# Kernel optimization log

Hardware: AMD Instinct MI355X
Metric: run time of the kernel (lower is better)

Reference implementation:

```python
import jax, jax.numpy as jnp
import numpy as np

N = 50000      # nodes
E = 1600000    # edges (before self-loops)
IN = 128       # in_chnl
H = 2          # heads
C = 64         # out_chnl per head
NEG_SLOPE = 0.2


def setup_inputs() -> dict:
    key = jax.random.key(0)
    k1, k2, k3, k4, k5 = jax.random.split(key, 5)
    h_node = jax.random.normal(k1, (N, IN), dtype=jnp.float32)
    edge_index = jax.random.randint(k2, (2, E), 0, N, dtype=jnp.int32)
    s = 1.0 / np.sqrt(IN)
    W = (jax.random.normal(k3, (IN, H * C), dtype=jnp.float32) * s)
    att_src = jax.random.normal(k4, (H, C), dtype=jnp.float32) * s
    att_dst = jax.random.normal(k5, (H, C), dtype=jnp.float32) * s
    bias = jnp.zeros((H * C,), dtype=jnp.float32)
    return {"h_node": h_node, "edge_index": edge_index, "W": W,
            "att_src": att_src, "att_dst": att_dst, "bias": bias}


def reference(h_node, edge_index, W, att_src, att_dst, bias):
    # dropout is identity in eval mode
    src, dst = edge_index[0], edge_index[1]
    # PyG GATConv default: add self-loops
    loops = jnp.arange(N, dtype=src.dtype)
    src = jnp.concatenate([src, loops])
    dst = jnp.concatenate([dst, loops])

    x = (h_node @ W).reshape(N, H, C)              # [N,H,C] projected features
    a_s = jnp.sum(x * att_src, axis=-1)            # [N,H] source attention terms
    a_d = jnp.sum(x * att_dst, axis=-1)            # [N,H] dest attention terms

    e = jax.nn.leaky_relu(a_s[src] + a_d[dst], NEG_SLOPE)        # [E+N,H]
    # segment softmax over edges grouped by destination node
    m = jax.lax.stop_gradient(jax.ops.segment_max(e, dst, num_segments=N))
    ex = jnp.exp(e - m[dst])
    den = jax.ops.segment_sum(ex, dst, num_segments=N)           # [N,H]
    alpha = ex / den[dst]                                        # [E+N,H]

    out = jax.ops.segment_sum(alpha[:, :, None] * x[src], dst, num_segments=N)
    out = out.reshape(N, H * C) + bias             # concat=True -> [N, H*C]
    return jax.nn.elu(out)
```

## Files before the change

kernel.cpp:

```cpp
#include <hip/hip_runtime.h>
#include <hip/hip_fp16.h>

#define NN 50000
#define EE 1600000
#define TOT (EE + NN)
#define INC 128
#define HC 128
#define NEG_SLOPE 0.2f

#define EPB 4096
#define NB1 ((TOT + EPB - 1) / EPB)
#define RNG2 64
#define NR2 ((NN + RNG2 - 1) / RNG2)
#define CAPR2 2624
#define PADC (CAPR2 + 4 * RNG2)
#define PROJB ((NN + 63) / 64)

__device__ __forceinline__ unsigned short f2h(float f) {
    __half h = __float2half(f);
    return __half_as_ushort(h);
}

__device__ __forceinline__ unsigned int packp(float a, float b) {
    typedef __fp16 h2 __attribute__((ext_vector_type(2)));
    union { h2 h; unsigned int u; } cv;
    cv.h = __builtin_amdgcn_cvt_pkrtz(a, b);
    return cv.u;
}

#define LOADW(dst, kk)                                                        \
    _Pragma("unroll") for (int q = 0; q < 4; q++) {                           \
        float4 wv4 = *reinterpret_cast<const float4*>(&W[(size_t)((kk) + q) * HC + j2 * 4]); \
        dst[q][0] = wv4.x; dst[q][1] = wv4.y; dst[q][2] = wv4.z; dst[q][3] = wv4.w; \
    }

#define FMAS(wv, kk)                                                          \
    _Pragma("unroll") for (int r8 = 0; r8 < 8; r8++) {                        \
        const float* hr = hs + (rg * 8 + r8) * INC + (kk);                    \
        float4 hv = *reinterpret_cast<const float4*>(hr);                     \
        _Pragma("unroll") for (int c = 0; c < 4; c++)                         \
            acc[r8][c] += hv.x * wv[0][c] + hv.y * wv[1][c]                   \
                        + hv.z * wv[2][c] + hv.w * wv[3][c];                  \
    }

__device__ __forceinline__ void proj_body(
        char* smem, int pb,
        const float* __restrict__ h, const float* __restrict__ W,
        const float* __restrict__ att_src, const float* __restrict__ att_dst,
        unsigned short* __restrict__ x_h,
        float* __restrict__ a_s, float* __restrict__ a_d) {
    float* hs = (float*)smem;
    const int t = threadIdx.x;
    const int row0 = pb * 64;

    for (int q = t; q < 64 * 32; q += 256) {
        int rr = q >> 5;
        int c4 = (q & 31) << 2;
        int gr = row0 + rr;
        float4 v = (gr < NN) ? *reinterpret_cast<const float4*>(&h[(size_t)gr * INC + c4])
                             : make_float4(0.f, 0.f, 0.f, 0.f);
        *reinterpret_cast<float4*>(&hs[rr * INC + c4]) = v;
    }
    __syncthreads();

    const int j2 = t & 31;
    const int rg = t >> 5;
    float acc[8][4];
#pragma unroll
    for (int r8 = 0; r8 < 8; r8++)
#pragma unroll
        for (int c = 0; c < 4; c++) acc[r8][c] = 0.f;

    float wA[4][4], wB[4][4];
    LOADW(wA, 0)
    for (int k = 0; k < INC; k += 8) {
        LOADW(wB, k + 4)
        FMAS(wA, k)
        if (k + 8 < INC) { LOADW(wA, k + 8) }
        FMAS(wB, k + 4)
    }

#pragma unroll
    for (int r8 = 0; r8 < 8; r8++) {
        int gr = row0 + rg * 8 + r8;
        if (gr < NN) {
            ushort4 sv;
            sv.x = f2h(acc[r8][0]);
            sv.y = f2h(acc[r8][1]);
            sv.z = f2h(acc[r8][2]);
            sv.w = f2h(acc[r8][3]);
            *reinterpret_cast<ushort4*>(&x_h[(size_t)gr * HC + j2 * 4]) = sv;
        }
    }

    const int lane = t & 63;
    const int hidx = j2 >> 4;
    const float4 avs = *reinterpret_cast<const float4*>(&att_src[j2 * 4]);
    const float4 avd = *reinterpret_cast<const float4*>(&att_dst[j2 * 4]);
#pragma unroll
    for (int r8 = 0; r8 < 8; r8++) {
        float ps = acc[r8][0] * avs.x + acc[r8][1] * avs.y
                 + acc[r8][2] * avs.z + acc[r8][3] * avs.w;
        float pd = acc[r8][0] * avd.x + acc[r8][1] * avd.y
                 + acc[r8][2] * avd.z + acc[r8][3] * avd.w;
#pragma unroll
        for (int o = 1; o < 16; o <<= 1) {
            ps += __shfl_xor(ps, o);
            pd += __shfl_xor(pd, o);
        }
        int gr = row0 + rg * 8 + r8;
        if ((lane & 15) == 0 && gr < NN) {
            a_s[gr * 2 + hidx] = ps;
            a_d[gr * 2 + hidx] = pd;
        }
    }
}

__device__ __forceinline__ void bin_body(
        char* smem, int b,
        const int* __restrict__ ei,
        unsigned int* __restrict__ gbin, unsigned short* __restrict__ bofs) {
    int* cnt = (int*)smem;
    int* ofs = cnt + NR2;
    int* cur = ofs + NR2 + 1;
    int* wsum = cur + NR2;
    unsigned int* lbuf = (unsigned int*)(wsum + 4);
    const int t = threadIdx.x;

    for (int i = t; i < NR2; i += 256) cnt[i] = 0;
    __syncthreads();

    unsigned int pk[16];
    bool vd[16];
#pragma unroll
    for (int q = 0; q < 16; q++) {
        int i = b * EPB + q * 256 + t;
        vd[q] = (i < TOT);
        int s, d;
        if (i < EE)       { s = ei[i]; d = ei[EE + i]; }
        else if (i < TOT) { s = d = i - EE; }
        else              { s = d = 0; }
        pk[q] = ((unsigned int)(d >> 6) << 22) |
                ((unsigned int)(d & 63) << 16) | (unsigned int)s;
        if (vd[q]) atomicAdd(&cnt[pk[q] >> 22], 1);
    }
    __syncthreads();

    {
        int i0 = 4 * t;
        int v0 = (i0     < NR2) ? cnt[i0]     : 0;
        int v1 = (i0 + 1 < NR2) ? cnt[i0 + 1] : 0;
        int v2 = (i0 + 2 < NR2) ? cnt[i0 + 2] : 0;
        int v3 = (i0 + 3 < NR2) ? cnt[i0 + 3] : 0;
        int ps = v0 + v1 + v2 + v3;
        int sc = ps;
        int lane = t & 63, wid = t >> 6;
#pragma unroll
        for (int o = 1; o < 64; o <<= 1) {
            int u = __shfl_up(sc, o);
            if (lane >= o) sc += u;
        }
        if (lane == 63) wsum[wid] = sc;
        __syncthreads();
        int woff = 0;
        for (int ww = 0; ww < wid; ww++) woff += wsum[ww];
        int run = woff + sc - ps;
        if (i0     <= NR2) ofs[i0]     = run; if (i0     < NR2) cur[i0]     = run; run += v0;
        if (i0 + 1 <= NR2) ofs[i0 + 1] = run; if (i0 + 1 < NR2) cur[i0 + 1] = run; run += v1;
        if (i0 + 2 <= NR2) ofs[i0 + 2] = run; if (i0 + 2 < NR2) cur[i0 + 2] = run; run += v2;
        if (i0 + 3 <= NR2) ofs[i0 + 3] = run; if (i0 + 3 < NR2) cur[i0 + 3] = run;
    }
    __syncthreads();

#pragma unroll
    for (int q = 0; q < 16; q++) {
        if (vd[q]) {
            int pos = atomicAdd(&cur[pk[q] >> 22], 1);
            lbuf[pos] = pk[q];
        }
    }
    __syncthreads();

#pragma unroll
    for (int q = 0; q < 16; q++)
        gbin[(size_t)b * EPB + q * 256 + t] = lbuf[q * 256 + t];
    for (int i = t; i <= NR2; i += 256)
        bofs[(size_t)b * (NR2 + 1) + i] = (unsigned short)ofs[i];
}

__global__ __launch_bounds__(256) void gat_fused1(
        const float* __restrict__ h, const float* __restrict__ W,
        const float* __restrict__ att_src, const float* __restrict__ att_dst,
        const int* __restrict__ ei,
        unsigned int* __restrict__ gbin, unsigned short* __restrict__ bofs,
        unsigned short* __restrict__ x_h,
        float* __restrict__ a_s, float* __restrict__ a_d) {
    __shared__ __align__(16) char smem[64 * INC * 4];
    if (blockIdx.x < NB1)
        bin_body(smem, blockIdx.x, ei, gbin, bofs);
    else
        proj_body(smem, blockIdx.x - NB1, h, W, att_src, att_dst, x_h, a_s, a_d);
}

#define ACCUM(u32v, aL, aH)                                                   \
    asm("v_fma_mix_f32 %0, %1, %2, %0 op_sel_hi:[0,1,0]"                      \
        : "+v"(aL) : "v"(wk), "v"(u32v));                                     \
    asm("v_fma_mix_f32 %0, %1, %2, %0 op_sel:[0,1,0] op_sel_hi:[0,1,0]"       \
        : "+v"(aH) : "v"(wk), "v"(u32v));

__global__ __launch_bounds__(512) void gat_ragg(
        const unsigned int* __restrict__ gbin,
        const unsigned short* __restrict__ bofs,
        const uint4* __restrict__ x16,
        const float2* __restrict__ a_s2, const float2* __restrict__ a_d2,
        const float4* __restrict__ bias4, float4* __restrict__ out4) {
    __shared__ int sbase[512];
    __shared__ int segofs[NB1];
    __shared__ unsigned short esrc[CAPR2];
    __shared__ unsigned char  edst[CAPR2];
    __shared__ unsigned int   pvh[CAPR2];
    __shared__ unsigned short csrc[PADC];
    __shared__ unsigned int   cpv[PADC];
    __shared__ int deg[RNG2];
    __shared__ int ofsP[RNG2];
    __shared__ int cur[RNG2];
    __shared__ int wsum[8];
    __shared__ int tot_sh;

    const int t = threadIdx.x;
    const int r = blockIdx.x;
    const int lane = t & 63, wid = t >> 6;

    if (t < RNG2) { deg[t] = 0; cur[t] = 0; }

    int c = 0;
    if (t < NB1) {
        int o0 = (int)bofs[(size_t)t * (NR2 + 1) + r];
        int o1 = (int)bofs[(size_t)t * (NR2 + 1) + r + 1];
        c = o1 - o0;
        segofs[t] = o0;
    }
    int sc = c;
#pragma unroll
    for (int o = 1; o < 64; o <<= 1) {
        int u = __shfl_up(sc, o);
        if (lane >= o) sc += u;
    }
    if (lane == 63) wsum[wid] = sc;
    __syncthreads();
    int woff = 0;
    for (int ww = 0; ww < wid; ww++) woff += wsum[ww];
    int excl = woff + sc - c;
    sbase[t] = excl;
    if (t == 511) tot_sh = excl + c;
    __syncthreads();
    const int tot = min(tot_sh, CAPR2);

    const float2* __restrict__ adr = a_d2 + (size_t)r * RNG2;
    for (int e = t; e < tot; e += 512) {
        int lo = 0, hi = NB1 - 1;
        while (lo < hi) {
            int mid = (lo + hi + 1) >> 1;
            if (sbase[mid] <= e) lo = mid; else hi = mid - 1;
        }
        unsigned int v = gbin[(size_t)lo * EPB + segofs[lo] + (e - sbase[lo])];
        int s  = (int)(v & 0xFFFFu);
        int dl = (int)((v >> 16) & 63u);
        esrc[e] = (unsigned short)s;
        edst[e] = (unsigned char)dl;
        float2 as = a_s2[s];
        float2 ad = adr[dl];
        float e0 = as.x + ad.x; e0 = (e0 > 0.f) ? e0 : NEG_SLOPE * e0;
        float e1 = as.y + ad.y; e1 = (e1 > 0.f) ? e1 : NEG_SLOPE * e1;
        pvh[e] = packp(__expf(e0), __expf(e1));
        atomicAdd(&deg[dl], 1);
    }
    __syncthreads();

    if (t < RNG2) {
        int v = deg[t];
        int s2 = v;
#pragma unroll
        for (int o = 1; o < 64; o <<= 1) {
            int u = __shfl_up(s2, o);
            if (lane >= o) s2 += u;
        }
        ofsP[t] = (s2 - v) + 4 * t;
    }
    __syncthreads();

    for (int e = t; e < tot; e += 512) {
        int dl = edst[e];
        int slot = ofsP[dl] + atomicAdd(&cur[dl], 1);
        csrc[slot] = esrc[e];
        cpv[slot]  = pvh[e];
    }
    if (t < RNG2 * 4) {
        int j = t >> 2, q = t & 3;
        int slot = ofsP[j] + deg[j] + q;
        csrc[slot] = 0;
        cpv[slot] = 0;
    }
    __syncthreads();

    const int sub = lane >> 4;
    const int cl  = lane & 15;
    const int hd  = cl >> 3;
    const int hsh = hd << 4;
    for (int jl = wid; jl < RNG2; jl += 8) {
        int n = r * RNG2 + jl;
        if (n >= NN) continue;
        const int dj = deg[jl];
        const int w0 = ofsP[jl];

        float d0 = 0.f, d1 = 0.f;
        for (int jj = lane; jj < dj; jj += 64) {
            unsigned int ph = cpv[w0 + jj];
            d0 += __half2float(__ushort_as_half((unsigned short)ph));
            d1 += __half2float(__ushort_as_half((unsigned short)(ph >> 16)));
        }
#pragma unroll
        for (int off = 32; off; off >>= 1) {
            d0 += __shfl_xor(d0, off);
            d1 += __shfl_xor(d1, off);
        }

        float a0=0.f,a1=0.f,a2=0.f,a3=0.f,a4=0.f,a5=0.f,a6=0.f,a7=0.f;
        const int ng = (dj + 3) >> 2;
        int g = 0;
        for (; g + 4 <= ng; g += 4) {
#pragma unroll
            for (int k = 0; k < 4; k++) {
                int e = 4 * (g + k) + sub;
                int s = (int)csrc[w0 + e];
                unsigned int ph = cpv[w0 + e];
                float wk = __half2float(__ushort_as_half((unsigned short)(ph >> hsh)));
                uint4 u = x16[(size_t)s * 16 + cl];
                ACCUM(u.x, a0, a1)
                ACCUM(u.y, a2, a3)
                ACCUM(u.z, a4, a5)
                ACCUM(u.w, a6, a7)
            }
        }
        for (; g < ng; g++) {
            int e = 4 * g + sub;
            int s = (int)csrc[w0 + e];
            unsigned int ph = cpv[w0 + e];
            float wk = __half2float(__ushort_as_half((unsigned short)(ph >> hsh)));
            uint4 u = x16[(size_t)s * 16 + cl];
            ACCUM(u.x, a0, a1)
            ACCUM(u.y, a2, a3)
            ACCUM(u.z, a4, a5)
            ACCUM(u.w, a6, a7)
        }
#define MRG(a) a += __shfl_xor(a, 16); a += __shfl_xor(a, 32);
        MRG(a0) MRG(a1) MRG(a2) MRG(a3) MRG(a4) MRG(a5) MRG(a6) MRG(a7)
#undef MRG

        if (lane < 32) {
            const int hf = lane >> 4;
            const float invd = 1.0f / (hd ? d1 : d0);
            float4 bb = bias4[cl * 2 + hf];
            float v0 = (hf ? a4 : a0) * invd + bb.x;
            float v1 = (hf ? a5 : a1) * invd + bb.y;
            float v2 = (hf ? a6 : a2) * invd + bb.z;
            float v3 = (hf ? a7 : a3) * invd + bb.w;
            v0 = (v0 > 0.f) ? v0 : __expf(v0) - 1.0f;
            v1 = (v1 > 0.f) ? v1 : __expf(v1) - 1.0f;
            v2 = (v2 > 0.f) ? v2 : __expf(v2) - 1.0f;
            v3 = (v3 > 0.f) ? v3 : __expf(v3) - 1.0f;
            out4[(size_t)n * 32 + cl * 2 + hf] = make_float4(v0, v1, v2, v3);
        }
    }
}

static inline size_t align256(size_t v) { return (v + 255) & ~(size_t)255; }

extern "C" void kernel_launch(void* const* d_in, const int* in_sizes, int n_in,
                              void* d_out, int out_size, void* d_ws, size_t ws_size,
                              hipStream_t stream) {
    const float* h_node  = (const float*)d_in[0];
    const int*   ei      = (const int*)d_in[1];
    const float* W       = (const float*)d_in[2];
    const float* att_src = (const float*)d_in[3];
    const float* att_dst = (const float*)d_in[4];
    const float* bias    = (const float*)d_in[5];
    float* out = (float*)d_out;

    char* base = (char*)d_ws;
    size_t off = 0;
    unsigned short* x_h = (unsigned short*)(base + off);
    off = align256(off + (size_t)NN * HC * 2);
    float* a_s = (float*)(base + off);      off = align256(off + (size_t)NN * 2 * 4);
    float* a_d = (float*)(base + off);      off = align256(off + (size_t)NN * 2 * 4);
    unsigned int* gbin = (unsigned int*)(base + off);
    off = align256(off + (size_t)NB1 * EPB * 4);
    unsigned short* bofs = (unsigned short*)(base + off);
    off = align256(off + (size_t)NB1 * (NR2 + 1) * 2);
    (void)ws_size;

    gat_fused1<<<NB1 + PROJB, 256, 0, stream>>>(h_node, W, att_src, att_dst, ei,
                                                gbin, bofs, x_h, a_s, a_d);
    gat_ragg<<<NR2, 512, 0, stream>>>(gbin, bofs, (const uint4*)x_h,
                                      (const float2*)a_s, (const float2*)a_d,
                                      (const float4*)bias, (float4*)out);
}
```

Measured before the change: 187.5 us.

## Compute node projection with fp16 MFMA using a swizzled transposed W tile in LDS

Replaces the scalar FP32 FMA projection (h @ W) with 16x16x32 fp16 MFMA instructions. Each block transposes W into LDS as fp16 with an XOR swizzle, and each wave loads its h rows directly into A fragments. Attention logits are then reduced from the MFMA accumulator layout. The cost is rebuilding W in LDS for every block and rounding h and W to fp16, which lowers precision, and the x_h stores become scattered 2-byte writes.

```diff
diff --git a/kernel.cpp b/kernel.cpp
--- a/kernel.cpp
+++ b/kernel.cpp
@@ -16,6 +16,9 @@
 #define PADC (CAPR2 + 4 * RNG2)
 #define PROJB ((NN + 63) / 64)
 
+typedef __fp16 h8 __attribute__((ext_vector_type(8)));
+typedef float f32x4v __attribute__((ext_vector_type(4)));
+
 __device__ __forceinline__ unsigned short f2h(float f) {
     __half h = __float2half(f);
     return __half_as_ushort(h);
@@ -27,21 +30,6 @@
     cv.h = __builtin_amdgcn_cvt_pkrtz(a, b);
     return cv.u;
 }
-
-#define LOADW(dst, kk)                                                        \
-    _Pragma("unroll") for (int q = 0; q < 4; q++) {                           \
-        float4 wv4 = *reinterpret_cast<const float4*>(&W[(size_t)((kk) + q) * HC + j2 * 4]); \
-        dst[q][0] = wv4.x; dst[q][1] = wv4.y; dst[q][2] = wv4.z; dst[q][3] = wv4.w; \
-    }
-
-#define FMAS(wv, kk)                                                          \
-    _Pragma("unroll") for (int r8 = 0; r8 < 8; r8++) {                        \
-        const float* hr = hs + (rg * 8 + r8) * INC + (kk);                    \
-        float4 hv = *reinterpret_cast<const float4*>(hr);                     \
-        _Pragma("unroll") for (int c = 0; c < 4; c++)                         \
-            acc[r8][c] += hv.x * wv[0][c] + hv.y * wv[1][c]                   \
-                        + hv.z * wv[2][c] + hv.w * wv[3][c];                  \
-    }
 
 __device__ __forceinline__ void proj_body(
         char* smem, int pb,
@@ -49,69 +37,96 @@
         const float* __restrict__ att_src, const float* __restrict__ att_dst,
         unsigned short* __restrict__ x_h,
         float* __restrict__ a_s, float* __restrict__ a_d) {
-    float* hs = (float*)smem;
+    unsigned short* Wt = (unsigned short*)smem;
     const int t = threadIdx.x;
+    const int w = t >> 6;
+    const int lane = t & 63;
+    const int l15 = lane & 15;
+    const int lg  = lane >> 4;
     const int row0 = pb * 64;
 
-    for (int q = t; q < 64 * 32; q += 256) {
-        int rr = q >> 5;
-        int c4 = (q & 31) << 2;
-        int gr = row0 + rr;
-        float4 v = (gr < NN) ? *reinterpret_cast<const float4*>(&h[(size_t)gr * INC + c4])
-                             : make_float4(0.f, 0.f, 0.f, 0.f);
-        *reinterpret_cast<float4*>(&hs[rr * INC + c4]) = v;
-    }
-    __syncthreads();
-
-    const int j2 = t & 31;
-    const int rg = t >> 5;
-    float acc[8][4];
-#pragma unroll
-    for (int r8 = 0; r8 < 8; r8++)
-#pragma unroll
-        for (int c = 0; c < 4; c++) acc[r8][c] = 0.f;
-
-    float wA[4][4], wB[4][4];
-    LOADW(wA, 0)
-    for (int k = 0; k < INC; k += 8) {
-        LOADW(wB, k + 4)
-        FMAS(wA, k)
-        if (k + 8 < INC) { LOADW(wA, k + 8) }
-        FMAS(wB, k + 4)
-    }
-
-#pragma unroll
-    for (int r8 = 0; r8 < 8; r8++) {
-        int gr = row0 + rg * 8 + r8;
-        if (gr < NN) {
-            ushort4 sv;
-            sv.x = f2h(acc[r8][0]);
-            sv.y = f2h(acc[r8][1]);
-            sv.z = f2h(acc[r8][2]);
-            sv.w = f2h(acc[r8][3]);
-            *reinterpret_cast<ushort4*>(&x_h[(size_t)gr * HC + j2 * 4]) = sv;
-        }
-    }
-
-    const int lane = t & 63;
-    const int hidx = j2 >> 4;
-    const float4 avs = *reinterpret_cast<const float4*>(&att_src[j2 * 4]);
-    const float4 avd = *reinterpret_cast<const float4*>(&att_dst[j2 * 4]);
-#pragma unroll
-    for (int r8 = 0; r8 < 8; r8++) {
-        float ps = acc[r8][0] * avs.x + acc[r8][1] * avs.y
-                 + acc[r8][2] * avs.z + acc[r8][3] * avs.w;
-        float pd = acc[r8][0] * avd.x + acc[r8][1] * avd.y
-                 + acc[r8][2] * avd.z + acc[r8][3] * avd.w;
+    for (int idx = t; idx < INC * HC; idx += 256) {
+        int k = idx & 127;
+        int c = idx >> 7;
+        float wv = W[(size_t)k * HC + c];
+        int byte = ((c * 128 + k) * 2) ^ ((c & 7) << 4);
+        Wt[byte >> 1] = f2h(wv);
+    }
+    __syncthreads();
+
+    const int arow = row0 + (w << 4) + l15;
+    const bool av = arow < NN;
+    const float* hrow = h + (size_t)arow * INC;
+    h8 afr[4];
+#pragma unroll
+    for (int ks = 0; ks < 4; ks++) {
+        int k0 = ks * 32 + (lg << 3);
+        float4 f0 = av ? *reinterpret_cast<const float4*>(hrow + k0)
+                       : make_float4(0.f, 0.f, 0.f, 0.f);
+        float4 f1 = av ? *reinterpret_cast<const float4*>(hrow + k0 + 4)
+                       : make_float4(0.f, 0.f, 0.f, 0.f);
+        h8 a;
+        a[0] = (__fp16)f0.x; a[1] = (__fp16)f0.y;
+        a[2] = (__fp16)f0.z; a[3] = (__fp16)f0.w;
+        a[4] = (__fp16)f1.x; a[5] = (__fp16)f1.y;
+        a[6] = (__fp16)f1.z; a[7] = (__fp16)f1.w;
+        afr[ks] = a;
+    }
+
+    f32x4v acc[8];
+#pragma unroll
+    for (int ct = 0; ct < 8; ct++) acc[ct] = (f32x4v){0.f, 0.f, 0.f, 0.f};
+#pragma unroll
+    for (int ks = 0; ks < 4; ks++) {
+        int kk = ks * 32 + (lg << 3);
+#pragma unroll
+        for (int ct = 0; ct < 8; ct++) {
+            int col = ct * 16 + l15;
+            int byte = ((col * 128 + kk) * 2) ^ ((col & 7) << 4);
+            h8 b = *reinterpret_cast<const h8*>(reinterpret_cast<const char*>(Wt) + byte);
+            acc[ct] = __builtin_amdgcn_mfma_f32_16x16x32_f16(afr[ks], b, acc[ct], 0, 0, 0);
+        }
+    }
+
+#pragma unroll
+    for (int reg = 0; reg < 4; reg++) {
+        int grow = row0 + (w << 4) + (lg << 2) + reg;
+        if (grow < NN) {
+#pragma unroll
+            for (int ct = 0; ct < 8; ct++)
+                x_h[(size_t)grow * HC + ct * 16 + l15] = f2h(acc[ct][reg]);
+        }
+    }
+
+    float AS[8], AD[8];
+#pragma unroll
+    for (int ct = 0; ct < 8; ct++) {
+        AS[ct] = att_src[ct * 16 + l15];
+        AD[ct] = att_dst[ct * 16 + l15];
+    }
+#pragma unroll
+    for (int reg = 0; reg < 4; reg++) {
+        float ps0 = 0.f, ps1 = 0.f, pd0 = 0.f, pd1 = 0.f;
+#pragma unroll
+        for (int ct = 0; ct < 4; ct++) {
+            ps0 += acc[ct][reg] * AS[ct];
+            pd0 += acc[ct][reg] * AD[ct];
+            ps1 += acc[ct + 4][reg] * AS[ct + 4];
+            pd1 += acc[ct + 4][reg] * AD[ct + 4];
+        }
 #pragma unroll
         for (int o = 1; o < 16; o <<= 1) {
-            ps += __shfl_xor(ps, o);
-            pd += __shfl_xor(pd, o);
-        }
-        int gr = row0 + rg * 8 + r8;
-        if ((lane & 15) == 0 && gr < NN) {
-            a_s[gr * 2 + hidx] = ps;
-            a_d[gr * 2 + hidx] = pd;
+            ps0 += __shfl_xor(ps0, o);
+            ps1 += __shfl_xor(ps1, o);
+            pd0 += __shfl_xor(pd0, o);
+            pd1 += __shfl_xor(pd1, o);
+        }
+        int grow = row0 + (w << 4) + (lg << 2) + reg;
+        if (l15 == 0 && grow < NN) {
+            a_s[grow * 2]     = ps0;
+            a_s[grow * 2 + 1] = ps1;
+            a_d[grow * 2]     = pd0;
+            a_d[grow * 2 + 1] = pd1;
         }
     }
 }
@@ -195,7 +210,7 @@
         unsigned int* __restrict__ gbin, unsigned short* __restrict__ bofs,
         unsigned short* __restrict__ x_h,
         float* __restrict__ a_s, float* __restrict__ a_d) {
-    __shared__ __align__(16) char smem[64 * INC * 4];
+    __shared__ __align__(16) char smem[INC * HC * 2];
     if (blockIdx.x < NB1)
         bin_body(smem, blockIdx.x, ei, gbin, bofs);
     else
```

After: 193.8 us. +3.4%, slower.
